# Kernel optimization log

Hardware: AMD Instinct MI355X
Metric: run time of the kernel (lower is better)

The kernel has to match this reference:

```python
import jax, jax.numpy as jnp
import numpy as np

N = 50000    # nodes
E = 800000   # edges
F = 128      # node_feature_dim
H = 128      # GCN hidden
H2 = 64      # fc1 hidden
T = 8        # num_tactics
G = 64       # graphs in batch


def setup_inputs() -> dict:
    key = jax.random.key(0)
    ks = jax.random.split(key, 12)
    s = 0.05
    return {
        "x": jax.random.normal(ks[0], (N, F), jnp.float32),
        "edge_index": jax.random.randint(ks[1], (2, E), 0, N, dtype=jnp.int32),
        "batch": jnp.sort(jax.random.randint(ks[2], (N,), 0, G, dtype=jnp.int32)),
        "W": jax.random.normal(ks[3], (F, H), jnp.float32) * s,
        "b": jax.random.normal(ks[4], (H,), jnp.float32) * s,
        "fc1_w": jax.random.normal(ks[5], (H, H2), jnp.float32) * s,
        "fc1_b": jax.random.normal(ks[6], (H2,), jnp.float32) * s,
        "actor_w": jax.random.normal(ks[7], (H2, T), jnp.float32) * s,
        "actor_b": jax.random.normal(ks[8], (T,), jnp.float32) * s,
        "critic_w": jax.random.normal(ks[9], (H2, 1), jnp.float32) * s,
        "critic_b": jax.random.normal(ks[10], (1,), jnp.float32) * s,
    }


def _gcn_conv(x, edge_index, W, b):
    # PyG GCNConv: add self-loops, symmetric D^-1/2 (A+I) D^-1/2 normalization,
    # linear transform first, then scatter-add aggregation, then bias.
    n = x.shape[0]
    loops = jnp.arange(n, dtype=edge_index.dtype)
    src = jnp.concatenate([edge_index[0], loops])  # message sources (x_j)
    dst = jnp.concatenate([edge_index[1], loops])  # aggregation targets
    deg = jax.ops.segment_sum(jnp.ones_like(dst, jnp.float32), dst, num_segments=N)
    dinv = deg ** -0.5  # deg >= 1 due to self-loops
    norm = dinv[src] * dinv[dst]                   # [E+N]
    h = x @ W                                      # [N, H]
    msgs = h[src] * norm[:, None]                  # [E+N, H]
    return jax.ops.segment_sum(msgs, dst, num_segments=N) + b


def reference(x, edge_index, batch, W, b, fc1_w, fc1_b, actor_w, actor_b, critic_w, critic_b):
    h = jax.nn.relu(_gcn_conv(x, edge_index, W, b))            # [N, H]
    # global_mean_pool over batch index
    sums = jax.ops.segment_sum(h, batch, num_segments=G)       # [G, H]
    cnts = jax.ops.segment_sum(jnp.ones((h.shape[0],), h.dtype), batch, num_segments=G)
    group_state = sums / jnp.maximum(cnts, 1.0)[:, None]
    z = jax.nn.relu(group_state @ fc1_w + fc1_b)               # [G, H2]
    tactic_probs = jax.nn.softmax(z @ actor_w + actor_b, axis=-1)  # [G, T]
    group_value = z @ critic_w + critic_b                      # [G, 1]
    return tactic_probs, group_value
```

## Files before the change

kernel.cpp:

```cpp
#include <hip/hip_runtime.h>
#include <hip/hip_bf16.h>

#define NN 50000
#define EE 800000
#define FF 128
#define HH 128
#define HID2 64
#define TT 8
#define GG 64
#define NB 196
#define NSB 256
#define EPB (EE / NSB)
#define NPAD 50048
#define SLAB4 ((size_t)NN * 4)
#define ANB 391

using frag_ab = __attribute__((ext_vector_type(8))) short;
using frag_cd = __attribute__((ext_vector_type(4))) float;

__device__ inline unsigned short f2bf(float f) {
    union { float f; unsigned u; } v; v.f = f;
    unsigned r = v.u + 0x7fff + ((v.u >> 16) & 1);
    return (unsigned short)(r >> 16);
}

__global__ __launch_bounds__(256) void k_front(const int* __restrict__ dst,
                                               const float* __restrict__ W,
                                               int* __restrict__ table,
                                               unsigned short* __restrict__ wt_bf,
                                               float* __restrict__ gsum) {
    __shared__ int cnt[4 * NB];
    int t = threadIdx.x, blk = blockIdx.x;
    int wv = t >> 6;
    if (blk < 64) {
        int gid = blk * 256 + t;
        int c = gid >> 7, k = gid & 127;
        wt_bf[gid] = f2bf(W[k * 128 + c]);
    }
    if (blk >= 64 && blk < 96) {
        int gid = (blk - 64) * 256 + t;
        gsum[gid] = 0.f;
    }
    for (int i = t; i < 4 * NB; i += 256) cnt[i] = 0;
    __syncthreads();
    int e0 = blk * EPB;
    int* my = cnt + wv * NB;
    for (int e = e0 + t; e < e0 + EPB; e += 256)
        atomicAdd(&my[dst[e] >> 8], 1);
    __syncthreads();
    for (int i = t; i < NB; i += 256)
        table[blk * NB + i] = cnt[i] + cnt[NB + i] + cnt[2 * NB + i] + cnt[3 * NB + i];
}

__global__ __launch_bounds__(256) void kb2a(int* __restrict__ table,
                                            int* __restrict__ ctot) {
    __shared__ int s[256];
    int t = threadIdx.x, b = blockIdx.x;
    int v = table[t * NB + b];
    s[t] = v;
    __syncthreads();
    for (int off = 1; off < 256; off <<= 1) {
        int a = s[t];
        int w = (t >= off) ? s[t - off] : 0;
        __syncthreads();
        s[t] = a + w;
        __syncthreads();
    }
    table[t * NB + b] = s[t] - v;
    if (t == 255) ctot[b] = s[255];
}

__global__ __launch_bounds__(256) void kb2b(const int* __restrict__ ctot,
                                            int* __restrict__ bbase) {
    __shared__ int s[256];
    int b = threadIdx.x;
    int v = (b < NB) ? ctot[b] : 0;
    s[b] = v;
    __syncthreads();
    for (int off = 1; off < 256; off <<= 1) {
        int a = s[b];
        int w = (b >= off) ? s[b - off] : 0;
        __syncthreads();
        s[b] = a + w;
        __syncthreads();
    }
    if (b < NB) bbase[b] = s[b] - v;
    if (b == 0) bbase[NB] = EE;
}

__global__ __launch_bounds__(256) void kb3(const int* __restrict__ src,
                                           const int* __restrict__ dst,
                                           const int* __restrict__ table,
                                           const int* __restrict__ bbase,
                                           unsigned* __restrict__ etmp) {
    __shared__ int ofs[NB];
    __shared__ int cur[NB];
    int t = threadIdx.x, blk = blockIdx.x;
    for (int i = t; i < NB; i += 256) {
        ofs[i] = table[blk * NB + i] + bbase[i];
        cur[i] = 0;
    }
    __syncthreads();
    int e0 = blk * EPB;
    for (int e = e0 + t; e < e0 + EPB; e += 256) {
        int d = dst[e];
        int b = d >> 8;
        int r = atomicAdd(&cur[b], 1);
        etmp[ofs[b] + r] = ((unsigned)d << 16) | (unsigned)src[e];
    }
}

__global__ __launch_bounds__(256) void k_csr(const unsigned* __restrict__ etmp,
                                             const int* __restrict__ bbase,
                                             int* __restrict__ row_ptr,
                                             float* __restrict__ dinv,
                                             unsigned short* __restrict__ srcs) {
    __shared__ int s[256];
    __shared__ int cur[256];
    int t = threadIdx.x, b = blockIdx.x;
    s[t] = 0;
    __syncthreads();
    int e0 = bbase[b], e1 = bbase[b + 1];
    for (int e = e0 + t; e < e1; e += 256)
        atomicAdd(&s[(etmp[e] >> 16) & 255], 1);
    __syncthreads();
    int v = s[t];
    for (int off = 1; off < 256; off <<= 1) {
        int a = s[t];
        int w = (t >= off) ? s[t - off] : 0;
        __syncthreads();
        s[t] = a + w;
        __syncthreads();
    }
    int excl = s[t] - v + e0;
    int node = b * 256 + t;
    if (node < NN) {
        row_ptr[node] = excl;
        dinv[node] = rsqrtf((float)(v + 1));
    }
    if (b == NB - 1 && t == 0) row_ptr[NN] = EE;
    cur[t] = excl;
    __syncthreads();
    for (int e = e0 + t; e < e1; e += 256) {
        unsigned u = etmp[e];
        int slot = atomicAdd(&cur[(u >> 16) & 255], 1);
        srcs[slot] = (unsigned short)(u & 0xffffu);
    }
}

__global__ __launch_bounds__(256) void k_gemm(const float* __restrict__ x,
                                              const unsigned short* __restrict__ wt_bf,
                                              const float* __restrict__ dinv,
                                              unsigned short* __restrict__ hsq) {
    int tid = threadIdx.x;
    int w = tid >> 6, lane = tid & 63;
    int m = lane & 15, quad = lane >> 4;
    int r0 = blockIdx.x * 64 + w * 16;
    int row = r0 + m;
    frag_cd acc[8];
#pragma unroll
    for (int nt = 0; nt < 8; nt++) acc[nt] = frag_cd{0.f, 0.f, 0.f, 0.f};

#pragma unroll
    for (int k0 = 0; k0 < 128; k0 += 32) {
        unsigned short av[8];
        if (row < NN) {
            const float4* p = (const float4*)(x + (size_t)row * 128 + k0 + quad * 8);
            float4 a0 = p[0], a1 = p[1];
            av[0] = f2bf(a0.x); av[1] = f2bf(a0.y); av[2] = f2bf(a0.z); av[3] = f2bf(a0.w);
            av[4] = f2bf(a1.x); av[5] = f2bf(a1.y); av[6] = f2bf(a1.z); av[7] = f2bf(a1.w);
        } else {
#pragma unroll
            for (int j = 0; j < 8; j++) av[j] = 0;
        }
        frag_ab a = *(const frag_ab*)av;
#pragma unroll
        for (int nt = 0; nt < 8; nt++) {
            frag_ab bfr = *(const frag_ab*)(wt_bf + (size_t)(nt * 16 + m) * 128 + k0 + quad * 8);
            acc[nt] = __builtin_amdgcn_mfma_f32_16x16x32_bf16(a, bfr, acc[nt], 0, 0, 0);
        }
    }
#pragma unroll
    for (int reg = 0; reg < 4; reg++) {
        int gr = r0 + quad * 4 + reg;
        if (gr < NN) {
            float di = dinv[gr];
#pragma unroll
            for (int nt = 0; nt < 8; nt++) {
                int c = nt * 16 + m;
                hsq[(size_t)(c >> 5) * (SLAB4 * 8) + (size_t)gr * 32 + (c & 31)] =
                    f2bf(acc[nt][reg] * di);
            }
        }
    }
}

#define ACC8(u) \
    a0 += __uint_as_float((u).x << 16); a1 += __uint_as_float((u).x & 0xffff0000u); \
    a2 += __uint_as_float((u).y << 16); a3 += __uint_as_float((u).y & 0xffff0000u); \
    a4 += __uint_as_float((u).z << 16); a5 += __uint_as_float((u).z & 0xffff0000u); \
    a6 += __uint_as_float((u).w << 16); a7 += __uint_as_float((u).w & 0xffff0000u);

__global__ __launch_bounds__(256) void k_aggr(const uint4* __restrict__ hsq4,
                                              const int* __restrict__ row_ptr,
                                              const unsigned short* __restrict__ srcs,
                                              const float* __restrict__ dinv,
                                              const float* __restrict__ bias,
                                              const int* __restrict__ batch,
                                              float* __restrict__ gsum) {
    __shared__ float gacc[8 * 32];
    int t = threadIdx.x;
    int q = blockIdx.x & 3;
    int nb = blockIdx.x >> 2;
    int grp = t >> 2, j = t & 3;
    int i_base = nb * 128;
    int last = i_base + 127; if (last >= NN) last = NN - 1;
    int g_first = batch[i_base];
    int gspan = batch[last] - g_first + 1;
    bool lds_pool = (gspan <= 8);
    int slots = lds_pool ? gspan : 0;
    if (t < slots * 32) gacc[t] = 0.f;
    __syncthreads();

    const uint4* slab4 = hsq4 + (size_t)q * SLAB4;
    const float4* b4 = (const float4*)(bias + q * 32 + j * 8);
    float4 bb0 = b4[0], bb1 = b4[1];

    for (int n = 0; n < 2; n++) {
        int i = i_base + grp * 2 + n;
        if (i >= NN) break;
        float di = dinv[i];
        uint4 su = slab4[(size_t)i * 4 + j];
        float a0 = __uint_as_float(su.x << 16);
        float a1 = __uint_as_float(su.x & 0xffff0000u);
        float a2 = __uint_as_float(su.y << 16);
        float a3 = __uint_as_float(su.y & 0xffff0000u);
        float a4 = __uint_as_float(su.z << 16);
        float a5 = __uint_as_float(su.z & 0xffff0000u);
        float a6 = __uint_as_float(su.w << 16);
        float a7 = __uint_as_float(su.w & 0xffff0000u);
        int e = row_ptr[i], e1 = row_ptr[i + 1];
        for (; e + 3 < e1; e += 4) {
            int s0 = srcs[e], s1 = srcs[e + 1], s2 = srcs[e + 2], s3 = srcs[e + 3];
            uint4 u0 = slab4[(size_t)s0 * 4 + j];
            uint4 u1 = slab4[(size_t)s1 * 4 + j];
            uint4 u2 = slab4[(size_t)s2 * 4 + j];
            uint4 u3 = slab4[(size_t)s3 * 4 + j];
            ACC8(u0) ACC8(u1) ACC8(u2) ACC8(u3)
        }
        for (; e < e1; ++e) {
            uint4 u0 = slab4[(size_t)srcs[e] * 4 + j];
            ACC8(u0)
        }
        float r0 = fmaxf(fmaf(a0, di, bb0.x), 0.f);
        float r1 = fmaxf(fmaf(a1, di, bb0.y), 0.f);
        float r2 = fmaxf(fmaf(a2, di, bb0.z), 0.f);
        float r3 = fmaxf(fmaf(a3, di, bb0.w), 0.f);
        float r4 = fmaxf(fmaf(a4, di, bb1.x), 0.f);
        float r5 = fmaxf(fmaf(a5, di, bb1.y), 0.f);
        float r6 = fmaxf(fmaf(a6, di, bb1.z), 0.f);
        float r7 = fmaxf(fmaf(a7, di, bb1.w), 0.f);
        int lg = batch[i] - g_first;
        float* gp = lds_pool ? &gacc[lg * 32 + j * 8]
                             : &gsum[(g_first + lg) * 128 + q * 32 + j * 8];
        atomicAdd(&gp[0], r0); atomicAdd(&gp[1], r1);
        atomicAdd(&gp[2], r2); atomicAdd(&gp[3], r3);
        atomicAdd(&gp[4], r4); atomicAdd(&gp[5], r5);
        atomicAdd(&gp[6], r6); atomicAdd(&gp[7], r7);
    }
    __syncthreads();
    if (t < slots * 32) {
        float v = gacc[t];
        if (v != 0.f)
            atomicAdd(&gsum[(g_first + (t >> 5)) * 128 + q * 32 + (t & 31)], v);
    }
}

__device__ inline int lbound(const int* __restrict__ a, int n, int key) {
    int lo = 0, hi = n;
    while (lo < hi) {
        int mid = (lo + hi) >> 1;
        if (a[mid] < key) lo = mid + 1;
        else hi = mid;
    }
    return lo;
}

__global__ __launch_bounds__(64) void k_head(const float* __restrict__ gsum,
                                             const int* __restrict__ batch,
                                             const float* __restrict__ fc1_w,
                                             const float* __restrict__ fc1_b,
                                             const float* __restrict__ actor_w,
                                             const float* __restrict__ actor_b,
                                             const float* __restrict__ critic_w,
                                             const float* __restrict__ critic_b,
                                             float* __restrict__ out) {
    __shared__ float gs[128];
    __shared__ float zs[64];
    __shared__ float ls[8], es[8];
    int g = blockIdx.x, t = threadIdx.x;
    int lo = lbound(batch, NN, g), hi = lbound(batch, NN, g + 1);
    float invc = 1.f / fmaxf((float)(hi - lo), 1.f);
    gs[t] = gsum[g * 128 + t] * invc;
    gs[t + 64] = gsum[g * 128 + 64 + t] * invc;
    __syncthreads();
    float z = fc1_b[t];
    for (int k = 0; k < 128; k++) z = fmaf(gs[k], fc1_w[k * 64 + t], z);
    zs[t] = fmaxf(z, 0.f);
    __syncthreads();
    if (t < 8) {
        float l = actor_b[t];
        for (int k = 0; k < 64; k++) l = fmaf(zs[k], actor_w[k * 8 + t], l);
        ls[t] = l;
    }
    __syncthreads();
    if (t < 8) {
        float m = ls[0];
#pragma unroll
        for (int j = 1; j < 8; j++) m = fmaxf(m, ls[j]);
        es[t] = expf(ls[t] - m);
    }
    __syncthreads();
    if (t < 8) {
        float ssum = 0.f;
#pragma unroll
        for (int j = 0; j < 8; j++) ssum += es[j];
        out[g * 8 + t] = es[t] / ssum;
    }
    if (t == 32) {
        float v = critic_b[0];
        for (int k = 0; k < 64; k++) v = fmaf(zs[k], critic_w[k], v);
        out[GG * TT + g] = v;
    }
}

extern "C" void kernel_launch(void* const* d_in, const int* in_sizes, int n_in,
                              void* d_out, int out_size, void* d_ws, size_t ws_size,
                              hipStream_t stream) {
    const float* x        = (const float*)d_in[0];
    const int*   ei       = (const int*)d_in[1];
    const int*   batch    = (const int*)d_in[2];
    const float* W        = (const float*)d_in[3];
    const float* b        = (const float*)d_in[4];
    const float* fc1_w    = (const float*)d_in[5];
    const float* fc1_b    = (const float*)d_in[6];
    const float* actor_w  = (const float*)d_in[7];
    const float* actor_b  = (const float*)d_in[8];
    const float* critic_w = (const float*)d_in[9];
    const float* critic_b = (const float*)d_in[10];
    float* out = (float*)d_out;

    char* ws = (char*)d_ws;
    size_t off = 0;
    unsigned short* hsq   = (unsigned short*)(ws + off); off += (size_t)NN * 128 * 2 + 64;
    unsigned short* wt_bf = (unsigned short*)(ws + off); off += (size_t)128 * 128 * 2;
    float* dinv      = (float*)(ws + off);    off += (size_t)NN * 4;
    int*   row_ptr   = (int*)(ws + off);      off += (size_t)(NN + 1) * 4 + 12;
    unsigned short* srcs = (unsigned short*)(ws + off); off += (size_t)EE * 2 + 32;
    unsigned* etmp   = (unsigned*)(ws + off); off += (size_t)EE * 4;
    int*   table     = (int*)(ws + off);      off += (size_t)NSB * NB * 4;
    int*   bbase     = (int*)(ws + off);      off += (size_t)(NB + 1) * 4 + 12;
    int*   ctot      = (int*)(ws + off);      off += (size_t)NB * 4 + 16;
    float* gsum      = (float*)(ws + off);    off += (size_t)GG * HH * 4;

    const int* src = ei;
    const int* dst = ei + EE;

    k_front<<<NSB, 256, 0, stream>>>(dst, W, table, wt_bf, gsum);
    kb2a<<<NB, 256, 0, stream>>>(table, ctot);
    kb2b<<<1, 256, 0, stream>>>(ctot, bbase);
    kb3<<<NSB, 256, 0, stream>>>(src, dst, table, bbase, etmp);
    k_csr<<<NB, 256, 0, stream>>>(etmp, bbase, row_ptr, dinv, srcs);
    k_gemm<<<NPAD / 64, 256, 0, stream>>>(x, wt_bf, dinv, hsq);
    k_aggr<<<ANB * 4, 256, 0, stream>>>((const uint4*)hsq, row_ptr, srcs,
                                        dinv, b, batch, gsum);
    k_head<<<GG, 64, 0, stream>>>(gsum, batch, fc1_w, fc1_b, actor_w, actor_b,
                                  critic_w, critic_b, out);
}
```

Baseline: 201.1 us.

## Balance aggregation by splitting edges evenly across thread groups with LDS accumulation

The aggregation kernel now assigns each block 64 nodes and splits that block's edge range evenly across 64 thread groups. This replaces the earlier one-thread-group-per-node loop, so load no longer depends on node degree. Partial sums are flushed into an LDS buffer with atomics, and self-loop, bias, ReLU and pooling are applied afterwards. The GEMM epilogue also writes a permuted column layout so each lane stores 8 contiguous bf16 values, and the pooling column index is remapped to match. The cost is more LDS atomics, a binary search per thread group and twice as many blocks.

```diff
diff --git a/kernel.cpp b/kernel.cpp
--- a/kernel.cpp
+++ b/kernel.cpp
@@ -12,8 +12,7 @@
 #define NSB 256
 #define EPB (EE / NSB)
 #define NPAD 50048
-#define SLAB4 ((size_t)NN * 4)
-#define ANB 391
+#define AGRP 782
 
 using frag_ab = __attribute__((ext_vector_type(8))) short;
 using frag_cd = __attribute__((ext_vector_type(4))) float;
@@ -180,17 +179,16 @@
             acc[nt] = __builtin_amdgcn_mfma_f32_16x16x32_bf16(a, bfr, acc[nt], 0, 0, 0);
         }
     }
+    unsigned short* slab = hsq + (size_t)(m >> 2) * ((size_t)NPAD * 32);
+    int ji = (m & 3) * 8;
 #pragma unroll
     for (int reg = 0; reg < 4; reg++) {
         int gr = r0 + quad * 4 + reg;
         if (gr < NN) {
             float di = dinv[gr];
 #pragma unroll
-            for (int nt = 0; nt < 8; nt++) {
-                int c = nt * 16 + m;
-                hsq[(size_t)(c >> 5) * (SLAB4 * 8) + (size_t)gr * 32 + (c & 31)] =
-                    f2bf(acc[nt][reg] * di);
-            }
+            for (int nt = 0; nt < 8; nt++)
+                slab[(size_t)gr * 32 + ji + nt] = f2bf(acc[nt][reg] * di);
         }
     }
 }
@@ -208,71 +206,83 @@
                                               const float* __restrict__ bias,
                                               const int* __restrict__ batch,
                                               float* __restrict__ gsum) {
-    __shared__ float gacc[8 * 32];
+    __shared__ int rptr[65];
+    __shared__ float gacc[64 * 36];
+    __shared__ float gpool[8 * 32];
     int t = threadIdx.x;
     int q = blockIdx.x & 3;
-    int nb = blockIdx.x >> 2;
-    int grp = t >> 2, j = t & 3;
-    int i_base = nb * 128;
-    int last = i_base + 127; if (last >= NN) last = NN - 1;
-    int g_first = batch[i_base];
-    int gspan = batch[last] - g_first + 1;
+    int grp = blockIdx.x >> 2;
+    int n0 = grp * 64;
+    int lg = t >> 2, j = t & 3;
+    if (t <= 64) {
+        int nd = n0 + t;
+        rptr[t] = row_ptr[nd > NN ? NN : nd];
+    }
+    for (int i = t; i < 64 * 36; i += 256) gacc[i] = 0.f;
+    int lastn = n0 + 63; if (lastn >= NN) lastn = NN - 1;
+    int g_first = batch[n0];
+    int gspan = batch[lastn] - g_first + 1;
     bool lds_pool = (gspan <= 8);
     int slots = lds_pool ? gspan : 0;
-    if (t < slots * 32) gacc[t] = 0.f;
-    __syncthreads();
-
-    const uint4* slab4 = hsq4 + (size_t)q * SLAB4;
-    const float4* b4 = (const float4*)(bias + q * 32 + j * 8);
-    float4 bb0 = b4[0], bb1 = b4[1];
-
-    for (int n = 0; n < 2; n++) {
-        int i = i_base + grp * 2 + n;
-        if (i >= NN) break;
-        float di = dinv[i];
-        uint4 su = slab4[(size_t)i * 4 + j];
-        float a0 = __uint_as_float(su.x << 16);
-        float a1 = __uint_as_float(su.x & 0xffff0000u);
-        float a2 = __uint_as_float(su.y << 16);
-        float a3 = __uint_as_float(su.y & 0xffff0000u);
-        float a4 = __uint_as_float(su.z << 16);
-        float a5 = __uint_as_float(su.z & 0xffff0000u);
-        float a6 = __uint_as_float(su.w << 16);
-        float a7 = __uint_as_float(su.w & 0xffff0000u);
-        int e = row_ptr[i], e1 = row_ptr[i + 1];
-        for (; e + 3 < e1; e += 4) {
-            int s0 = srcs[e], s1 = srcs[e + 1], s2 = srcs[e + 2], s3 = srcs[e + 3];
-            uint4 u0 = slab4[(size_t)s0 * 4 + j];
-            uint4 u1 = slab4[(size_t)s1 * 4 + j];
-            uint4 u2 = slab4[(size_t)s2 * 4 + j];
-            uint4 u3 = slab4[(size_t)s3 * 4 + j];
-            ACC8(u0) ACC8(u1) ACC8(u2) ACC8(u3)
-        }
-        for (; e < e1; ++e) {
-            uint4 u0 = slab4[(size_t)srcs[e] * 4 + j];
-            ACC8(u0)
-        }
-        float r0 = fmaxf(fmaf(a0, di, bb0.x), 0.f);
-        float r1 = fmaxf(fmaf(a1, di, bb0.y), 0.f);
-        float r2 = fmaxf(fmaf(a2, di, bb0.z), 0.f);
-        float r3 = fmaxf(fmaf(a3, di, bb0.w), 0.f);
-        float r4 = fmaxf(fmaf(a4, di, bb1.x), 0.f);
-        float r5 = fmaxf(fmaf(a5, di, bb1.y), 0.f);
-        float r6 = fmaxf(fmaf(a6, di, bb1.z), 0.f);
-        float r7 = fmaxf(fmaf(a7, di, bb1.w), 0.f);
-        int lg = batch[i] - g_first;
-        float* gp = lds_pool ? &gacc[lg * 32 + j * 8]
-                             : &gsum[(g_first + lg) * 128 + q * 32 + j * 8];
-        atomicAdd(&gp[0], r0); atomicAdd(&gp[1], r1);
-        atomicAdd(&gp[2], r2); atomicAdd(&gp[3], r3);
-        atomicAdd(&gp[4], r4); atomicAdd(&gp[5], r5);
-        atomicAdd(&gp[6], r6); atomicAdd(&gp[7], r7);
+    if (t < slots * 32) gpool[t] = 0.f;
+    __syncthreads();
+
+    const uint4* slab4 = hsq4 + (size_t)q * ((size_t)NPAD * 4);
+    int e0 = rptr[0], e1 = rptr[64];
+    int cnt = e1 - e0;
+    int per = (cnt + 63) >> 6;
+    int ce = e0 + lg * per;
+    int cend = ce + per; if (cend > e1) cend = e1;
+    if (ce < cend) {
+        int lo = 0, hi = 64;
+        while (lo + 1 < hi) {
+            int mid = (lo + hi) >> 1;
+            if (rptr[mid] <= ce) lo = mid; else hi = mid;
+        }
+        int d = lo;
+        float a0 = 0.f, a1 = 0.f, a2 = 0.f, a3 = 0.f,
+              a4 = 0.f, a5 = 0.f, a6 = 0.f, a7 = 0.f;
+        for (int e = ce; e < cend; ++e) {
+            int s = srcs[e];
+            uint4 u = slab4[(size_t)s * 4 + j];
+            ACC8(u)
+            int nx = e + 1;
+            if (nx == rptr[d + 1] || nx == cend) {
+                float* gp = &gacc[d * 36 + j * 8];
+                atomicAdd(&gp[0], a0); atomicAdd(&gp[1], a1);
+                atomicAdd(&gp[2], a2); atomicAdd(&gp[3], a3);
+                atomicAdd(&gp[4], a4); atomicAdd(&gp[5], a5);
+                atomicAdd(&gp[6], a6); atomicAdd(&gp[7], a7);
+                a0 = a1 = a2 = a3 = a4 = a5 = a6 = a7 = 0.f;
+                if (nx < cend) {
+                    while (rptr[d + 1] <= nx) d++;
+                }
+            }
+        }
+    }
+    __syncthreads();
+    const unsigned short* slab_us = (const unsigned short*)slab4;
+    for (int it = t; it < 64 * 32; it += 256) {
+        int n = it >> 5, idx = it & 31;
+        int node = n0 + n;
+        if (node < NN) {
+            int c = ((idx & 7) << 4) + q * 4 + (idx >> 3);
+            unsigned short sv = slab_us[(size_t)node * 32 + idx];
+            float self = __uint_as_float(((unsigned)sv) << 16);
+            float v = fmaf(gacc[n * 36 + idx] + self, dinv[node], bias[c]);
+            v = fmaxf(v, 0.f);
+            int g = batch[node];
+            if (lds_pool) atomicAdd(&gpool[(g - g_first) * 32 + idx], v);
+            else          atomicAdd(&gsum[g * 128 + c], v);
+        }
     }
     __syncthreads();
     if (t < slots * 32) {
-        float v = gacc[t];
+        float v = gpool[t];
+        int idx = t & 31;
+        int c = ((idx & 7) << 4) + q * 4 + (idx >> 3);
         if (v != 0.f)
-            atomicAdd(&gsum[(g_first + (t >> 5)) * 128 + q * 32 + (t & 31)], v);
+            atomicAdd(&gsum[(g_first + (t >> 5)) * 128 + c], v);
     }
 }
 
@@ -352,7 +362,7 @@
 
     char* ws = (char*)d_ws;
     size_t off = 0;
-    unsigned short* hsq   = (unsigned short*)(ws + off); off += (size_t)NN * 128 * 2 + 64;
+    unsigned short* hsq   = (unsigned short*)(ws + off); off += (size_t)NPAD * 128 * 2 + 64;
     unsigned short* wt_bf = (unsigned short*)(ws + off); off += (size_t)128 * 128 * 2;
     float* dinv      = (float*)(ws + off);    off += (size_t)NN * 4;
     int*   row_ptr   = (int*)(ws + off);      off += (size_t)(NN + 1) * 4 + 12;
@@ -372,8 +382,8 @@
     kb3<<<NSB, 256, 0, stream>>>(src, dst, table, bbase, etmp);
     k_csr<<<NB, 256, 0, stream>>>(etmp, bbase, row_ptr, dinv, srcs);
     k_gemm<<<NPAD / 64, 256, 0, stream>>>(x, wt_bf, dinv, hsq);
-    k_aggr<<<ANB * 4, 256, 0, stream>>>((const uint4*)hsq, row_ptr, srcs,
-                                        dinv, b, batch, gsum);
+    k_aggr<<<AGRP * 4, 256, 0, stream>>>((const uint4*)hsq, row_ptr, srcs,
+                                         dinv, b, batch, gsum);
     k_head<<<GG, 64, 0, stream>>>(gsum, batch, fc1_w, fc1_b, actor_w, actor_b,
                                   critic_w, critic_b, out);
 }
```

Result: slower. 257.6 us (+28.1%).
